# Optimization experiments

Measured on AMD Instinct MI355X. Metric: run time of the kernel, lower is better.

The kernel has to match this reference:

```python
import jax, jax.numpy as jnp
import numpy as np

WINDOW = 5  # must be odd so conv 'same' output length == tlength


def setup_inputs() -> dict:
    key = jax.random.key(0)
    tlength = 16777216
    return {"factor": jax.random.normal(key, (tlength,), dtype=jnp.float32)}


def reference(factor):
    window = WINDOW
    # moving average: conv1d with ones kernel, padding=window//2 (== 'same' for odd window)
    w = jnp.ones((window,), dtype=factor.dtype)
    moving_average = jnp.convolve(factor, w, mode='same') / window
    # rate of change: 0 followed by squared consecutive differences
    diffs = (moving_average[:-1] - moving_average[1:]) ** 2
    change = jnp.concatenate([jnp.zeros((1,), dtype=factor.dtype), diffs])
    change = change / jnp.sum(change)
    # power-weighted elementwise scaling
    return (1.0 - change) ** 5 * factor
```

## Files before the change

kernel.cpp:

```cpp
#include <hip/hip_runtime.h>


#define BLOCK 256
#define RGRID_MAX 2048

typedef __attribute__((ext_vector_type(4))) float vfloat4;

__device__ __forceinline__ float change_term(const float* __restrict__ f, long long i, long long n) {
    if (i < 1) return 0.0f;
    float a = (i >= 3)    ? f[i - 3] : 0.0f;
    float b = (i + 2 < n) ? f[i + 2] : 0.0f;
    float d = a - b;
    return d * d;
}

__device__ __forceinline__ float pow5(float t) {
    float t2 = t * t;
    float t4 = t2 * t2;
    return t4 * t;
}

__device__ __forceinline__ float vec_terms(float4 p, float4 c, float4 q) {
    float d0 = p.y - c.z;
    float d1 = p.z - c.w;
    float d2 = p.w - q.x;
    float d3 = c.x - q.y;
    return d0 * d0 + d1 * d1 + d2 * d2 + d3 * d3;
}

__device__ __forceinline__ vfloat4 vec_out(float4 p, float4 c, float4 q, float inv) {
    float d0 = p.y - c.z;
    float d1 = p.z - c.w;
    float d2 = p.w - q.x;
    float d3 = c.x - q.y;
    vfloat4 o;
    o.x = pow5(1.0f - d0 * d0 * inv) * c.x;
    o.y = pow5(1.0f - d1 * d1 * inv) * c.y;
    o.z = pow5(1.0f - d2 * d2 * inv) * c.z;
    o.w = pow5(1.0f - d3 * d3 * inv) * c.w;
    return o;
}

__global__ __launch_bounds__(BLOCK)
void reduce_change_kernel(const float* __restrict__ f, int nvec, long long n,
                          float* __restrict__ partials) {
    const float4* __restrict__ fv = (const float4*)f;
    const int T = gridDim.x * BLOCK;
    const int tid = blockIdx.x * BLOCK + threadIdx.x;
    const int M = nvec - 2;
    float acc = 0.0f;

    int idx = tid;
    for (; idx + 3 * T < M; idx += 4 * T) {
        float4 p[4], c[4], q[4];
        #pragma unroll
        for (int u = 0; u < 4; ++u) {
            int v = 1 + idx + u * T;
            p[u] = fv[v - 1];
            c[u] = fv[v];
            q[u] = fv[v + 1];
        }
        #pragma unroll
        for (int u = 0; u < 4; ++u)
            acc += vec_terms(p[u], c[u], q[u]);
    }
    for (; idx < M; idx += T) {
        int v = 1 + idx;
        acc += vec_terms(fv[v - 1], fv[v], fv[v + 1]);
    }
    if (tid == 0) {
        #pragma unroll
        for (int k = 0; k < 4; ++k) acc += change_term(f, k, n);
        long long j0 = n - 4;
        #pragma unroll
        for (int k = 0; k < 4; ++k) acc += change_term(f, j0 + k, n);
    }

    #pragma unroll
    for (int off = 32; off > 0; off >>= 1)
        acc += __shfl_down(acc, off, 64);
    __shared__ float smem[4];
    int lane = threadIdx.x & 63;
    int wave = threadIdx.x >> 6;
    if (lane == 0) smem[wave] = acc;
    __syncthreads();
    if (threadIdx.x == 0)
        partials[blockIdx.x] = smem[0] + smem[1] + smem[2] + smem[3];
}

__global__ __launch_bounds__(BLOCK)
void finalize_kernel(const float* __restrict__ f, int nvec, long long n,
                     const float* __restrict__ partials, int npart,
                     float* __restrict__ out) {
    const float4* __restrict__ fv = (const float4*)f;
    vfloat4* __restrict__ ov = (vfloat4*)out;
    const int M = nvec - 2;
    const int T = (M + 3) >> 2;
    const int tid = blockIdx.x * BLOCK + threadIdx.x;

    bool active = tid < T;
    int i0 = active ? tid : 0;
    bool ok1 = active && (i0 + 1 * T < M);
    bool ok2 = active && (i0 + 2 * T < M);
    bool ok3 = active && (i0 + 3 * T < M);
    int v0 = 1 + i0;
    int v1 = ok1 ? v0 + T : v0;
    int v2 = ok2 ? v1 + T : v1;
    int v3 = ok3 ? v2 + T : v2;
    float4 p0 = fv[v0 - 1], c0 = fv[v0], q0 = fv[v0 + 1];
    float4 p1 = fv[v1 - 1], c1 = fv[v1], q1 = fv[v1 + 1];
    float4 p2 = fv[v2 - 1], c2 = fv[v2], q2 = fv[v2 + 1];
    float4 p3 = fv[v3 - 1], c3 = fv[v3], q3 = fv[v3 + 1];

    float s = 0.0f;
    for (int k = threadIdx.x; k < npart; k += BLOCK)
        s += partials[k];
    #pragma unroll
    for (int off = 32; off > 0; off >>= 1)
        s += __shfl_down(s, off, 64);
    __shared__ float smem[4];
    __shared__ float stot;
    int lane = threadIdx.x & 63;
    int wave = threadIdx.x >> 6;
    if (lane == 0) smem[wave] = s;
    __syncthreads();
    if (threadIdx.x == 0) stot = smem[0] + smem[1] + smem[2] + smem[3];
    __syncthreads();
    float inv = 1.0f / stot;

    if (active) {
        __builtin_nontemporal_store(vec_out(p0, c0, q0, inv), &ov[v0]);
        if (ok1) __builtin_nontemporal_store(vec_out(p1, c1, q1, inv), &ov[v1]);
        if (ok2) __builtin_nontemporal_store(vec_out(p2, c2, q2, inv), &ov[v2]);
        if (ok3) __builtin_nontemporal_store(vec_out(p3, c3, q3, inv), &ov[v3]);
    }
    if (tid == 0) {
        #pragma unroll
        for (int k = 0; k < 4; ++k) {
            float cge = change_term(f, k, n) * inv;
            out[k] = pow5(1.0f - cge) * f[k];
        }
        long long j0 = n - 4;
        #pragma unroll
        for (int k = 0; k < 4; ++k) {
            long long j = j0 + k;
            float cge = change_term(f, j, n) * inv;
            out[j] = pow5(1.0f - cge) * f[j];
        }
    }
}

extern "C" void kernel_launch(void* const* d_in, const int* in_sizes, int n_in,
                              void* d_out, int out_size, void* d_ws, size_t ws_size,
                              hipStream_t stream) {
    const float* f = (const float*)d_in[0];
    float* out = (float*)d_out;
    float* partials = (float*)d_ws;
    long long n = (long long)in_sizes[0];
    int nvec = (int)(n / 4);

    int rgrid = RGRID_MAX;
    if (ws_size > 0 && (size_t)rgrid * sizeof(float) > ws_size) {
        rgrid = (int)(ws_size / sizeof(float));
        if (rgrid > RGRID_MAX) rgrid = RGRID_MAX;
        if (rgrid < 1) rgrid = 1;
    }

    reduce_change_kernel<<<rgrid, BLOCK, 0, stream>>>(f, nvec, n, partials);

    int M = nvec - 2;
    int T = (M + 3) >> 2;
    int fgrid = (T + BLOCK - 1) / BLOCK;
    finalize_kernel<<<fgrid, BLOCK, 0, stream>>>(f, nvec, n, partials, rgrid, out);
}
```

Baseline: 123.7 us.

## Fuse reduction and output pass into one cooperative kernel with grid sync

Replaces the two-kernel reduce+finalize pipeline with a single cooperative kernel that computes partial sums, performs a grid-wide sync, reduces partials, then rereads the input to write the scaled output. The aim is to remove the second launch and its tail gap. The grid is sized by occupancy and capped at 2048 blocks. It adds a grid-sync barrier cost, and because the grid is limited to resident blocks, the output pass becomes grid-stride instead of one-shot. The second input read may still partly hit cache.

New measurement: 234.2 us. +89.4%, slower.

```diff
diff --git a/kernel.cpp b/kernel.cpp
--- a/kernel.cpp
+++ b/kernel.cpp
@@ -1,8 +1,11 @@
 #include <hip/hip_runtime.h>
+#include <hip/hip_cooperative_groups.h>
+
+namespace cg = cooperative_groups;
 
 
 #define BLOCK 256
-#define RGRID_MAX 2048
+#define CGRID_MAX 2048
 
 typedef __attribute__((ext_vector_type(4))) float vfloat4;
 
@@ -41,6 +44,104 @@
     return o;
 }
 
+
+__global__ __launch_bounds__(BLOCK, 4)
+void fused_kernel(const float* __restrict__ f, int nvec, long long n,
+                  float* __restrict__ partials, float* __restrict__ out) {
+    const float4* __restrict__ fv = (const float4*)f;
+    vfloat4* __restrict__ ov = (vfloat4*)out;
+    const int T = gridDim.x * BLOCK;
+    const int tid = blockIdx.x * BLOCK + threadIdx.x;
+    const int M = nvec - 2;
+
+    float acc = 0.0f;
+    int idx = tid;
+    for (; idx + 3 * T < M; idx += 4 * T) {
+        float4 p[4], c[4], q[4];
+        #pragma unroll
+        for (int u = 0; u < 4; ++u) {
+            int v = 1 + idx + u * T;
+            p[u] = fv[v - 1];
+            c[u] = fv[v];
+            q[u] = fv[v + 1];
+        }
+        #pragma unroll
+        for (int u = 0; u < 4; ++u)
+            acc += vec_terms(p[u], c[u], q[u]);
+    }
+    for (; idx < M; idx += T) {
+        int v = 1 + idx;
+        acc += vec_terms(fv[v - 1], fv[v], fv[v + 1]);
+    }
+    if (tid == 0) {
+        #pragma unroll
+        for (int k = 0; k < 4; ++k) acc += change_term(f, k, n);
+        long long j0 = n - 4;
+        #pragma unroll
+        for (int k = 0; k < 4; ++k) acc += change_term(f, j0 + k, n);
+    }
+
+    #pragma unroll
+    for (int off = 32; off > 0; off >>= 1)
+        acc += __shfl_down(acc, off, 64);
+    __shared__ float smem[4];
+    __shared__ float stot;
+    int lane = threadIdx.x & 63;
+    int wave = threadIdx.x >> 6;
+    if (lane == 0) smem[wave] = acc;
+    __syncthreads();
+    if (threadIdx.x == 0)
+        partials[blockIdx.x] = smem[0] + smem[1] + smem[2] + smem[3];
+
+    cg::this_grid().sync();
+
+    float s = 0.0f;
+    for (int k = threadIdx.x; k < (int)gridDim.x; k += BLOCK)
+        s += partials[k];
+    #pragma unroll
+    for (int off = 32; off > 0; off >>= 1)
+        s += __shfl_down(s, off, 64);
+    if (lane == 0) smem[wave] = s;
+    __syncthreads();
+    if (threadIdx.x == 0) stot = smem[0] + smem[1] + smem[2] + smem[3];
+    __syncthreads();
+    const float inv = 1.0f / stot;
+
+    idx = tid;
+    for (; idx + 3 * T < M; idx += 4 * T) {
+        float4 p[4], c[4], q[4];
+        #pragma unroll
+        for (int u = 0; u < 4; ++u) {
+            int v = 1 + idx + u * T;
+            p[u] = fv[v - 1];
+            c[u] = fv[v];
+            q[u] = fv[v + 1];
+        }
+        #pragma unroll
+        for (int u = 0; u < 4; ++u)
+            __builtin_nontemporal_store(vec_out(p[u], c[u], q[u], inv), &ov[1 + idx + u * T]);
+    }
+    for (; idx < M; idx += T) {
+        int v = 1 + idx;
+        __builtin_nontemporal_store(vec_out(fv[v - 1], fv[v], fv[v + 1], inv), &ov[v]);
+    }
+    if (tid == 0) {
+        #pragma unroll
+        for (int k = 0; k < 4; ++k) {
+            float cge = change_term(f, k, n) * inv;
+            out[k] = pow5(1.0f - cge) * f[k];
+        }
+        long long j0 = n - 4;
+        #pragma unroll
+        for (int k = 0; k < 4; ++k) {
+            long long j = j0 + k;
+            float cge = change_term(f, j, n) * inv;
+            out[j] = pow5(1.0f - cge) * f[j];
+        }
+    }
+}
+
+
 __global__ __launch_bounds__(BLOCK)
 void reduce_change_kernel(const float* __restrict__ f, int nvec, long long n,
                           float* __restrict__ partials) {
@@ -49,7 +150,6 @@
     const int tid = blockIdx.x * BLOCK + threadIdx.x;
     const int M = nvec - 2;
     float acc = 0.0f;
-
     int idx = tid;
     for (; idx + 3 * T < M; idx += 4 * T) {
         float4 p[4], c[4], q[4];
@@ -75,7 +175,6 @@
         #pragma unroll
         for (int k = 0; k < 4; ++k) acc += change_term(f, j0 + k, n);
     }
-
     #pragma unroll
     for (int off = 32; off > 0; off >>= 1)
         acc += __shfl_down(acc, off, 64);
@@ -150,6 +249,7 @@
     }
 }
 
+
 extern "C" void kernel_launch(void* const* d_in, const int* in_sizes, int n_in,
                               void* d_out, int out_size, void* d_ws, size_t ws_size,
                               hipStream_t stream) {
@@ -159,15 +259,39 @@
     long long n = (long long)in_sizes[0];
     int nvec = (int)(n / 4);
 
-    int rgrid = RGRID_MAX;
-    if (ws_size > 0 && (size_t)rgrid * sizeof(float) > ws_size) {
-        rgrid = (int)(ws_size / sizeof(float));
-        if (rgrid > RGRID_MAX) rgrid = RGRID_MAX;
-        if (rgrid < 1) rgrid = 1;
-    }
-
+    static int coop_grid = -1;
+    static bool coop_ok = true;
+    if (coop_grid < 0) {
+        int dev = 0;
+        (void)hipGetDevice(&dev);
+        int ncu = 0;
+        if (hipDeviceGetAttribute(&ncu, hipDeviceAttributeMultiprocessorCount, dev) != hipSuccess || ncu <= 0)
+            ncu = 256;
+        int blocks_per_cu = 0;
+        if (hipOccupancyMaxActiveBlocksPerMultiprocessor(&blocks_per_cu, fused_kernel, BLOCK, 0) != hipSuccess
+            || blocks_per_cu <= 0) {
+            coop_ok = false;
+            blocks_per_cu = 1;
+        }
+        long long g = (long long)blocks_per_cu * ncu;
+        if (g > CGRID_MAX) g = CGRID_MAX;
+        if (ws_size > 0 && (size_t)g * sizeof(float) > ws_size)
+            g = (long long)(ws_size / sizeof(float));
+        if (g < 1) { g = 1; coop_ok = false; }
+        coop_grid = (int)g;
+    }
+
+    if (coop_ok) {
+        void* args[] = {(void*)&f, (void*)&nvec, (void*)&n, (void*)&partials, (void*)&out};
+        hipError_t err = hipLaunchCooperativeKernel((const void*)fused_kernel,
+                                                    dim3((unsigned)coop_grid), dim3(BLOCK),
+                                                    args, 0, stream);
+        if (err == hipSuccess) return;
+        coop_ok = false;
+    }
+
+    int rgrid = coop_grid > 0 ? coop_grid : 1024;
     reduce_change_kernel<<<rgrid, BLOCK, 0, stream>>>(f, nvec, n, partials);
-
     int M = nvec - 2;
     int T = (M + 3) >> 2;
     int fgrid = (T + BLOCK - 1) / BLOCK;
```

## Process 16 contiguous elements per thread to cut halo reloads

Applied to the files above, without the earlier changes.

Each thread now handles a contiguous group of four float4 vectors and loads one float4 halo on each side (6 loads for 16 outputs), replacing the old scheme of three float4 loads per output vector. This lowers redundant global/L2 traffic in both the reduction and the finalize kernel. Boundary handling grows to 16 elements at each end, done by 32 threads. Per-thread accesses become strided by 64 bytes across lanes, which may hurt coalescing compared with the previous layout.

Measured after the change: 188.2 us. +52.2%, slower.

```diff
diff --git a/kernel.cpp b/kernel.cpp
--- a/kernel.cpp
+++ b/kernel.cpp
@@ -20,60 +20,69 @@
     return t4 * t;
 }
 
-__device__ __forceinline__ float vec_terms(float4 p, float4 c, float4 q) {
-    float d0 = p.y - c.z;
-    float d1 = p.z - c.w;
-    float d2 = p.w - q.x;
-    float d3 = c.x - q.y;
-    return d0 * d0 + d1 * d1 + d2 * d2 + d3 * d3;
+__device__ __forceinline__ void unpack24(const float4* A, float* L) {
+    #pragma unroll
+    for (int u = 0; u < 6; ++u) {
+        L[4 * u + 0] = A[u].x;
+        L[4 * u + 1] = A[u].y;
+        L[4 * u + 2] = A[u].z;
+        L[4 * u + 3] = A[u].w;
+    }
 }
 
-__device__ __forceinline__ vfloat4 vec_out(float4 p, float4 c, float4 q, float inv) {
-    float d0 = p.y - c.z;
-    float d1 = p.z - c.w;
-    float d2 = p.w - q.x;
-    float d3 = c.x - q.y;
-    vfloat4 o;
-    o.x = pow5(1.0f - d0 * d0 * inv) * c.x;
-    o.y = pow5(1.0f - d1 * d1 * inv) * c.y;
-    o.z = pow5(1.0f - d2 * d2 * inv) * c.z;
-    o.w = pow5(1.0f - d3 * d3 * inv) * c.w;
-    return o;
+__device__ __forceinline__ float group_terms(const float4* A) {
+    float L[24];
+    unpack24(A, L);
+    float s = 0.0f;
+    #pragma unroll
+    for (int k = 0; k < 16; ++k) {
+        float d = L[k + 1] - L[k + 6];
+        s = fmaf(d, d, s);
+    }
+    return s;
 }
 
 __global__ __launch_bounds__(BLOCK)
 void reduce_change_kernel(const float* __restrict__ f, int nvec, long long n,
                           float* __restrict__ partials) {
     const float4* __restrict__ fv = (const float4*)f;
+    const int G = nvec >> 2;
+    const int NG = G - 2;
     const int T = gridDim.x * BLOCK;
     const int tid = blockIdx.x * BLOCK + threadIdx.x;
-    const int M = nvec - 2;
     float acc = 0.0f;
 
-    int idx = tid;
-    for (; idx + 3 * T < M; idx += 4 * T) {
-        float4 p[4], c[4], q[4];
+    int g = tid;
+    for (; g + T < NG; g += 2 * T) {
+        int i0 = 1 + g;
+        int i1 = 1 + g + T;
+        float4 A[6], B[6];
+        A[0] = fv[4 * i0 - 1];
+        B[0] = fv[4 * i1 - 1];
         #pragma unroll
         for (int u = 0; u < 4; ++u) {
-            int v = 1 + idx + u * T;
-            p[u] = fv[v - 1];
-            c[u] = fv[v];
-            q[u] = fv[v + 1];
+            A[1 + u] = fv[4 * i0 + u];
+            B[1 + u] = fv[4 * i1 + u];
         }
+        A[5] = fv[4 * i0 + 4];
+        B[5] = fv[4 * i1 + 4];
+        acc += group_terms(A);
+        acc += group_terms(B);
+    }
+    for (; g < NG; g += T) {
+        int i0 = 1 + g;
+        float4 A[6];
+        A[0] = fv[4 * i0 - 1];
         #pragma unroll
-        for (int u = 0; u < 4; ++u)
-            acc += vec_terms(p[u], c[u], q[u]);
+        for (int u = 0; u < 4; ++u) A[1 + u] = fv[4 * i0 + u];
+        A[5] = fv[4 * i0 + 4];
+        acc += group_terms(A);
     }
-    for (; idx < M; idx += T) {
-        int v = 1 + idx;
-        acc += vec_terms(fv[v - 1], fv[v], fv[v + 1]);
-    }
-    if (tid == 0) {
-        #pragma unroll
-        for (int k = 0; k < 4; ++k) acc += change_term(f, k, n);
-        long long j0 = n - 4;
-        #pragma unroll
-        for (int k = 0; k < 4; ++k) acc += change_term(f, j0 + k, n);
+
+    if (blockIdx.x == 0 && threadIdx.x < 32) {
+        long long j = (threadIdx.x < 16) ? (long long)threadIdx.x
+                                         : (n - 16 + (threadIdx.x - 16));
+        acc += change_term(f, j, n);
     }
 
     #pragma unroll
@@ -94,23 +103,17 @@
                      float* __restrict__ out) {
     const float4* __restrict__ fv = (const float4*)f;
     vfloat4* __restrict__ ov = (vfloat4*)out;
-    const int M = nvec - 2;
-    const int T = (M + 3) >> 2;
+    const int G = nvec >> 2;
+    const int NG = G - 2;
     const int tid = blockIdx.x * BLOCK + threadIdx.x;
 
-    bool active = tid < T;
-    int i0 = active ? tid : 0;
-    bool ok1 = active && (i0 + 1 * T < M);
-    bool ok2 = active && (i0 + 2 * T < M);
-    bool ok3 = active && (i0 + 3 * T < M);
-    int v0 = 1 + i0;
-    int v1 = ok1 ? v0 + T : v0;
-    int v2 = ok2 ? v1 + T : v1;
-    int v3 = ok3 ? v2 + T : v2;
-    float4 p0 = fv[v0 - 1], c0 = fv[v0], q0 = fv[v0 + 1];
-    float4 p1 = fv[v1 - 1], c1 = fv[v1], q1 = fv[v1 + 1];
-    float4 p2 = fv[v2 - 1], c2 = fv[v2], q2 = fv[v2 + 1];
-    float4 p3 = fv[v3 - 1], c3 = fv[v3], q3 = fv[v3 + 1];
+    bool active = tid < NG;
+    int i = 1 + (active ? tid : 0);
+    float4 A[6];
+    A[0] = fv[4 * i - 1];
+    #pragma unroll
+    for (int u = 0; u < 4; ++u) A[1 + u] = fv[4 * i + u];
+    A[5] = fv[4 * i + 4];
 
     float s = 0.0f;
     for (int k = threadIdx.x; k < npart; k += BLOCK)
@@ -126,27 +129,33 @@
     __syncthreads();
     if (threadIdx.x == 0) stot = smem[0] + smem[1] + smem[2] + smem[3];
     __syncthreads();
-    float inv = 1.0f / stot;
+    const float inv = 1.0f / stot;
 
     if (active) {
-        __builtin_nontemporal_store(vec_out(p0, c0, q0, inv), &ov[v0]);
-        if (ok1) __builtin_nontemporal_store(vec_out(p1, c1, q1, inv), &ov[v1]);
-        if (ok2) __builtin_nontemporal_store(vec_out(p2, c2, q2, inv), &ov[v2]);
-        if (ok3) __builtin_nontemporal_store(vec_out(p3, c3, q3, inv), &ov[v3]);
+        float L[24];
+        unpack24(A, L);
+        float o[16];
+        #pragma unroll
+        for (int k = 0; k < 16; ++k) {
+            float d = L[k + 1] - L[k + 6];
+            o[k] = pow5(1.0f - d * d * inv) * L[k + 4];
+        }
+        #pragma unroll
+        for (int u = 0; u < 4; ++u) {
+            vfloat4 v;
+            v.x = o[4 * u + 0];
+            v.y = o[4 * u + 1];
+            v.z = o[4 * u + 2];
+            v.w = o[4 * u + 3];
+            __builtin_nontemporal_store(v, &ov[4 * i + u]);
+        }
     }
-    if (tid == 0) {
-        #pragma unroll
-        for (int k = 0; k < 4; ++k) {
-            float cge = change_term(f, k, n) * inv;
-            out[k] = pow5(1.0f - cge) * f[k];
-        }
-        long long j0 = n - 4;
-        #pragma unroll
-        for (int k = 0; k < 4; ++k) {
-            long long j = j0 + k;
-            float cge = change_term(f, j, n) * inv;
-            out[j] = pow5(1.0f - cge) * f[j];
-        }
+
+    if (blockIdx.x == 0 && threadIdx.x < 32) {
+        long long j = (threadIdx.x < 16) ? (long long)threadIdx.x
+                                         : (n - 16 + (threadIdx.x - 16));
+        float cge = change_term(f, j, n) * inv;
+        out[j] = pow5(1.0f - cge) * f[j];
     }
 }
 
@@ -168,8 +177,8 @@
 
     reduce_change_kernel<<<rgrid, BLOCK, 0, stream>>>(f, nvec, n, partials);
 
-    int M = nvec - 2;
-    int T = (M + 3) >> 2;
-    int fgrid = (T + BLOCK - 1) / BLOCK;
+    int G = nvec >> 2;
+    int NG = G - 2;
+    int fgrid = (NG + BLOCK - 1) / BLOCK;
     finalize_kernel<<<fgrid, BLOCK, 0, stream>>>(f, nvec, n, partials, rgrid, out);
 }
```

## Stage contiguous chunks with halo in LDS to avoid triple-reading neighbors

Applied to the files above, without the earlier changes.

Both kernels now give each block a contiguous chunk of 2048 float4s plus a two-vector halo, loaded once into shared memory. Stencil neighbours are then read from LDS, where before each thread issued three overlapping global float4 loads. Boundary handling is folded into zero-padded loads and a v==0 check. The reduction now launches one block per chunk (about 2048 blocks), and the finalize kernel sums that many partials per block. In exchange, each block uses about 32 KB of LDS, which limits occupancy, and the launch ignores ws_size, so the partials buffer could overflow if the workspace is small.

After: 127.1 us. 2.7% more time.

```diff
diff --git a/kernel.cpp b/kernel.cpp
--- a/kernel.cpp
+++ b/kernel.cpp
@@ -2,17 +2,10 @@
 
 
 #define BLOCK 256
-#define RGRID_MAX 2048
+#define VPT 8
+#define VPB (BLOCK * VPT)
 
 typedef __attribute__((ext_vector_type(4))) float vfloat4;
-
-__device__ __forceinline__ float change_term(const float* __restrict__ f, long long i, long long n) {
-    if (i < 1) return 0.0f;
-    float a = (i >= 3)    ? f[i - 3] : 0.0f;
-    float b = (i + 2 < n) ? f[i + 2] : 0.0f;
-    float d = a - b;
-    return d * d;
-}
 
 __device__ __forceinline__ float pow5(float t) {
     float t2 = t * t;
@@ -20,132 +13,107 @@
     return t4 * t;
 }
 
-__device__ __forceinline__ float vec_terms(float4 p, float4 c, float4 q) {
-    float d0 = p.y - c.z;
-    float d1 = p.z - c.w;
-    float d2 = p.w - q.x;
-    float d3 = c.x - q.y;
-    return d0 * d0 + d1 * d1 + d2 * d2 + d3 * d3;
-}
-
-__device__ __forceinline__ vfloat4 vec_out(float4 p, float4 c, float4 q, float inv) {
-    float d0 = p.y - c.z;
-    float d1 = p.z - c.w;
-    float d2 = p.w - q.x;
-    float d3 = c.x - q.y;
-    vfloat4 o;
-    o.x = pow5(1.0f - d0 * d0 * inv) * c.x;
-    o.y = pow5(1.0f - d1 * d1 * inv) * c.y;
-    o.z = pow5(1.0f - d2 * d2 * inv) * c.z;
-    o.w = pow5(1.0f - d3 * d3 * inv) * c.w;
-    return o;
+__device__ __forceinline__ void stage_chunk(const float4* __restrict__ fv,
+                                            long long base, int nvec,
+                                            float4* __restrict__ lds, int t) {
+    #pragma unroll
+    for (int j = 0; j <= VPT; ++j) {
+        int h = t + j * BLOCK;
+        if (h < VPB + 2) {
+            long long v = base - 1 + h;
+            float4 val;
+            if (v >= 0 && v < (long long)nvec) {
+                val = fv[v];
+            } else {
+                val.x = 0.0f; val.y = 0.0f; val.z = 0.0f; val.w = 0.0f;
+            }
+            lds[h] = val;
+        }
+    }
 }
 
 __global__ __launch_bounds__(BLOCK)
-void reduce_change_kernel(const float* __restrict__ f, int nvec, long long n,
-                          float* __restrict__ partials) {
+void reduce_kernel(const float* __restrict__ f, int nvec,
+                   float* __restrict__ partials) {
+    __shared__ float4 lds[VPB + 2];
     const float4* __restrict__ fv = (const float4*)f;
-    const int T = gridDim.x * BLOCK;
-    const int tid = blockIdx.x * BLOCK + threadIdx.x;
-    const int M = nvec - 2;
+    const int t = threadIdx.x;
+    const long long base = (long long)blockIdx.x * VPB;
+
+    stage_chunk(fv, base, nvec, lds, t);
+    __syncthreads();
+
     float acc = 0.0f;
-
-    int idx = tid;
-    for (; idx + 3 * T < M; idx += 4 * T) {
-        float4 p[4], c[4], q[4];
-        #pragma unroll
-        for (int u = 0; u < 4; ++u) {
-            int v = 1 + idx + u * T;
-            p[u] = fv[v - 1];
-            c[u] = fv[v];
-            q[u] = fv[v + 1];
+    #pragma unroll
+    for (int j = 0; j < VPT; ++j) {
+        int h = 1 + t + j * BLOCK;
+        long long v = base + t + j * BLOCK;
+        if (v < (long long)nvec) {
+            float4 p = lds[h - 1], c = lds[h], q = lds[h + 1];
+            float d0 = p.y - c.z;
+            float d1 = p.z - c.w;
+            float d2 = p.w - q.x;
+            float d3 = c.x - q.y;
+            if (v == 0) d0 = 0.0f;
+            acc += d0 * d0 + d1 * d1 + d2 * d2 + d3 * d3;
         }
-        #pragma unroll
-        for (int u = 0; u < 4; ++u)
-            acc += vec_terms(p[u], c[u], q[u]);
-    }
-    for (; idx < M; idx += T) {
-        int v = 1 + idx;
-        acc += vec_terms(fv[v - 1], fv[v], fv[v + 1]);
-    }
-    if (tid == 0) {
-        #pragma unroll
-        for (int k = 0; k < 4; ++k) acc += change_term(f, k, n);
-        long long j0 = n - 4;
-        #pragma unroll
-        for (int k = 0; k < 4; ++k) acc += change_term(f, j0 + k, n);
     }
 
     #pragma unroll
     for (int off = 32; off > 0; off >>= 1)
         acc += __shfl_down(acc, off, 64);
     __shared__ float smem[4];
-    int lane = threadIdx.x & 63;
-    int wave = threadIdx.x >> 6;
+    const int lane = t & 63;
+    const int wave = t >> 6;
     if (lane == 0) smem[wave] = acc;
     __syncthreads();
-    if (threadIdx.x == 0)
+    if (t == 0)
         partials[blockIdx.x] = smem[0] + smem[1] + smem[2] + smem[3];
 }
 
 __global__ __launch_bounds__(BLOCK)
-void finalize_kernel(const float* __restrict__ f, int nvec, long long n,
+void finalize_kernel(const float* __restrict__ f, int nvec,
                      const float* __restrict__ partials, int npart,
                      float* __restrict__ out) {
+    __shared__ float4 lds[VPB + 2];
+    __shared__ float smem_s[4];
     const float4* __restrict__ fv = (const float4*)f;
     vfloat4* __restrict__ ov = (vfloat4*)out;
-    const int M = nvec - 2;
-    const int T = (M + 3) >> 2;
-    const int tid = blockIdx.x * BLOCK + threadIdx.x;
+    const int t = threadIdx.x;
+    const long long base = (long long)blockIdx.x * VPB;
 
-    bool active = tid < T;
-    int i0 = active ? tid : 0;
-    bool ok1 = active && (i0 + 1 * T < M);
-    bool ok2 = active && (i0 + 2 * T < M);
-    bool ok3 = active && (i0 + 3 * T < M);
-    int v0 = 1 + i0;
-    int v1 = ok1 ? v0 + T : v0;
-    int v2 = ok2 ? v1 + T : v1;
-    int v3 = ok3 ? v2 + T : v2;
-    float4 p0 = fv[v0 - 1], c0 = fv[v0], q0 = fv[v0 + 1];
-    float4 p1 = fv[v1 - 1], c1 = fv[v1], q1 = fv[v1 + 1];
-    float4 p2 = fv[v2 - 1], c2 = fv[v2], q2 = fv[v2 + 1];
-    float4 p3 = fv[v3 - 1], c3 = fv[v3], q3 = fv[v3 + 1];
+    stage_chunk(fv, base, nvec, lds, t);
 
     float s = 0.0f;
-    for (int k = threadIdx.x; k < npart; k += BLOCK)
+    for (int k = t; k < npart; k += BLOCK)
         s += partials[k];
     #pragma unroll
     for (int off = 32; off > 0; off >>= 1)
         s += __shfl_down(s, off, 64);
-    __shared__ float smem[4];
-    __shared__ float stot;
-    int lane = threadIdx.x & 63;
-    int wave = threadIdx.x >> 6;
-    if (lane == 0) smem[wave] = s;
+    const int lane = t & 63;
+    const int wave = t >> 6;
+    if (lane == 0) smem_s[wave] = s;
+
     __syncthreads();
-    if (threadIdx.x == 0) stot = smem[0] + smem[1] + smem[2] + smem[3];
-    __syncthreads();
-    float inv = 1.0f / stot;
+    const float inv = 1.0f / (smem_s[0] + smem_s[1] + smem_s[2] + smem_s[3]);
 
-    if (active) {
-        __builtin_nontemporal_store(vec_out(p0, c0, q0, inv), &ov[v0]);
-        if (ok1) __builtin_nontemporal_store(vec_out(p1, c1, q1, inv), &ov[v1]);
-        if (ok2) __builtin_nontemporal_store(vec_out(p2, c2, q2, inv), &ov[v2]);
-        if (ok3) __builtin_nontemporal_store(vec_out(p3, c3, q3, inv), &ov[v3]);
-    }
-    if (tid == 0) {
-        #pragma unroll
-        for (int k = 0; k < 4; ++k) {
-            float cge = change_term(f, k, n) * inv;
-            out[k] = pow5(1.0f - cge) * f[k];
-        }
-        long long j0 = n - 4;
-        #pragma unroll
-        for (int k = 0; k < 4; ++k) {
-            long long j = j0 + k;
-            float cge = change_term(f, j, n) * inv;
-            out[j] = pow5(1.0f - cge) * f[j];
+    #pragma unroll
+    for (int j = 0; j < VPT; ++j) {
+        int h = 1 + t + j * BLOCK;
+        long long v = base + t + j * BLOCK;
+        if (v < (long long)nvec) {
+            float4 p = lds[h - 1], c = lds[h], q = lds[h + 1];
+            float d0 = p.y - c.z;
+            float d1 = p.z - c.w;
+            float d2 = p.w - q.x;
+            float d3 = c.x - q.y;
+            if (v == 0) d0 = 0.0f;
+            vfloat4 o;
+            o.x = pow5(1.0f - d0 * d0 * inv) * c.x;
+            o.y = pow5(1.0f - d1 * d1 * inv) * c.y;
+            o.z = pow5(1.0f - d2 * d2 * inv) * c.z;
+            o.w = pow5(1.0f - d3 * d3 * inv) * c.w;
+            __builtin_nontemporal_store(o, &ov[v]);
         }
     }
 }
@@ -159,17 +127,8 @@
     long long n = (long long)in_sizes[0];
     int nvec = (int)(n / 4);
 
-    int rgrid = RGRID_MAX;
-    if (ws_size > 0 && (size_t)rgrid * sizeof(float) > ws_size) {
-        rgrid = (int)(ws_size / sizeof(float));
-        if (rgrid > RGRID_MAX) rgrid = RGRID_MAX;
-        if (rgrid < 1) rgrid = 1;
-    }
+    int grid = (nvec + VPB - 1) / VPB;
 
-    reduce_change_kernel<<<rgrid, BLOCK, 0, stream>>>(f, nvec, n, partials);
-
-    int M = nvec - 2;
-    int T = (M + 3) >> 2;
-    int fgrid = (T + BLOCK - 1) / BLOCK;
-    finalize_kernel<<<fgrid, BLOCK, 0, stream>>>(f, nvec, n, partials, rgrid, out);
+    reduce_kernel<<<grid, BLOCK, 0, stream>>>(f, nvec, partials);
+    finalize_kernel<<<grid, BLOCK, 0, stream>>>(f, nvec, partials, grid, out);
 }
```
